# Kernel tuning notes

Hardware: AMD Instinct MI355X
Metric: run time of the kernel (lower is better)

## Reference

```python
import jax, jax.numpy as jnp
import numpy as np

B, K = 16384, 32      # batch nodes, sampled neighbors per node
N, F, E = 1000000, 128, 128  # table size, feature_dim, embed_dim


def setup_inputs() -> dict:
    key = jax.random.key(0)
    k1, k2, k3 = jax.random.split(key, 3)
    id2feat = jax.random.normal(k1, (N, F), dtype=jnp.float32)
    # xavier_uniform for weight
    limit = float(np.sqrt(6.0 / (F + E)))
    weight = jax.random.uniform(k2, (F, E), dtype=jnp.float32, minval=-limit, maxval=limit)
    bias = jnp.zeros((E,), dtype=jnp.float32)
    neigh_idx = jax.random.randint(k3, (B, K), 0, N, dtype=jnp.int64)
    return {"id2feat": id2feat, "weight": weight, "bias": bias, "neigh_idx": neigh_idx}


def reference(id2feat, weight, bias, neigh_idx):
    # gather neighbor features: [B, K, F]
    feats = id2feat[neigh_idx]
    # linear transform then mean over neighbors (== mask.mm(embed_matrix))
    emb = jnp.einsum('bkf,fe->bke', feats, weight) + bias  # [B, K, E]
    return emb.mean(axis=1)  # [B, E]
```

## Files before the change

### kernel.cpp

```cpp
#include <hip/hip_runtime.h>


#define BATCH 16384
#define KNB   32
#define FDIM  128
#define EDIM  128
#define ROWS_PER_BLOCK 16
#define IDX_PITCH 33
#define A_PITCH  132

__global__ __launch_bounds__(256, 2)
void spa_agg_kernel(const float* __restrict__ id2feat,
                    const float* __restrict__ weight,
                    const float* __restrict__ bias,
                    const int* __restrict__ neigh_idx,
                    float* __restrict__ out) {
    __shared__ float sW[FDIM * EDIM];
    __shared__ float sA[ROWS_PER_BLOCK * A_PITCH];
    __shared__ int   sIdx[ROWS_PER_BLOCK * IDX_PITCH];

    const int tid = threadIdx.x;
    const int lb  = tid >> 4;
    const int fg  = tid & 15;
    const int b0  = blockIdx.x * ROWS_PER_BLOCK;

    {
        const int base = b0 * KNB;
        for (int i = tid; i < ROWS_PER_BLOCK * KNB; i += 256) {
            int r = i >> 5, c = i & 31;
            sIdx[r * IDX_PITCH + c] = neigh_idx[base + i];
        }
    }
    {
        for (int i = tid; i < (FDIM * EDIM) / 4; i += 256) {
            int f = i >> 5, e4 = i & 31;
            const float4 w = *(const float4*)(weight + (size_t)f * EDIM + e4 * 4);
            *(float4*)&sW[f * 128 + (e4 & 1) * 64 + (e4 >> 1) * 4] = w;
        }
    }
    __syncthreads();

    {
        float acc[8];
        #pragma unroll
        for (int j = 0; j < 8; ++j) acc[j] = 0.f;
        const int* ip = &sIdx[lb * IDX_PITCH];
        #pragma unroll 8
        for (int k = 0; k < KNB; ++k) {
            const int row = ip[k];
            const float4* rp = (const float4*)(id2feat + (size_t)row * FDIM + fg * 8);
            const float4 r0 = rp[0];
            const float4 r1 = rp[1];
            acc[0] += r0.x; acc[1] += r0.y; acc[2] += r0.z; acc[3] += r0.w;
            acc[4] += r1.x; acc[5] += r1.y; acc[6] += r1.z; acc[7] += r1.w;
        }
        float* ap = &sA[lb * A_PITCH + fg * 8];
        #pragma unroll
        for (int j = 0; j < 8; ++j) ap[j] = acc[j] * (1.f / 32.f);
    }
    __syncthreads();

    {
        const int e0 = fg * 8;
        float acc[8];
        #pragma unroll
        for (int j = 0; j < 8; ++j) acc[j] = bias[e0 + j];
        const float* arow = &sA[lb * A_PITCH];
        #pragma unroll 4
        for (int f = 0; f < FDIM; ++f) {
            const float a   = arow[f];
            const float4 w0 = *(const float4*)&sW[f * 128 + fg * 4];
            const float4 w1 = *(const float4*)&sW[f * 128 + 64 + fg * 4];
            acc[0] += a * w0.x; acc[1] += a * w0.y;
            acc[2] += a * w0.z; acc[3] += a * w0.w;
            acc[4] += a * w1.x; acc[5] += a * w1.y;
            acc[6] += a * w1.z; acc[7] += a * w1.w;
        }
        float* op = out + (size_t)(b0 + lb) * EDIM + e0;
        *(float4*)op       = make_float4(acc[0], acc[1], acc[2], acc[3]);
        *(float4*)(op + 4) = make_float4(acc[4], acc[5], acc[6], acc[7]);
    }
}

extern "C" void kernel_launch(void* const* d_in, const int* in_sizes, int n_in,
                              void* d_out, int out_size, void* d_ws, size_t ws_size,
                              hipStream_t stream) {
    const float* id2feat = (const float*)d_in[0];
    const float* weight  = (const float*)d_in[1];
    const float* bias    = (const float*)d_in[2];
    const int*   neigh   = (const int*)d_in[3];
    float*       outp    = (float*)d_out;

    dim3 grid(BATCH / ROWS_PER_BLOCK);
    dim3 block(256);
    spa_agg_kernel<<<grid, block, 0, stream>>>(id2feat, weight, bias, neigh, outp);
}
```

Measured before the change: 607.5 us.

## Drop shared weight staging and halve rows per block for higher occupancy

The 64 KB shared-memory copy of the weight matrix is removed, and the GEMV stage now reads weight rows straight from global memory through the cache. Rows per block drop to 8, and each warp of 32 threads handles one batch row with a float4 per lane. With shared memory nearly empty, the launch bounds now allow 6 blocks per CU, giving more loads in flight for the random gather. The cost is that every block reads the full weight from L2/L1 instead of LDS, and twice as many blocks are launched.

Result: no change. 614.1 us (+1.1%).

```diff
diff --git a/kernel.cpp b/kernel.cpp
--- a/kernel.cpp
+++ b/kernel.cpp
@@ -5,80 +5,59 @@
 #define KNB   32
 #define FDIM  128
 #define EDIM  128
-#define ROWS_PER_BLOCK 16
+#define ROWS_PER_BLOCK 8
 #define IDX_PITCH 33
 #define A_PITCH  132
 
-__global__ __launch_bounds__(256, 2)
+__global__ __launch_bounds__(256, 6)
 void spa_agg_kernel(const float* __restrict__ id2feat,
                     const float* __restrict__ weight,
                     const float* __restrict__ bias,
                     const int* __restrict__ neigh_idx,
                     float* __restrict__ out) {
-    __shared__ float sW[FDIM * EDIM];
     __shared__ float sA[ROWS_PER_BLOCK * A_PITCH];
     __shared__ int   sIdx[ROWS_PER_BLOCK * IDX_PITCH];
 
     const int tid = threadIdx.x;
-    const int lb  = tid >> 4;
-    const int fg  = tid & 15;
+    const int lr  = tid >> 5;
+    const int c   = tid & 31;
     const int b0  = blockIdx.x * ROWS_PER_BLOCK;
 
     {
-        const int base = b0 * KNB;
-        for (int i = tid; i < ROWS_PER_BLOCK * KNB; i += 256) {
-            int r = i >> 5, c = i & 31;
-            sIdx[r * IDX_PITCH + c] = neigh_idx[base + i];
-        }
-    }
-    {
-        for (int i = tid; i < (FDIM * EDIM) / 4; i += 256) {
-            int f = i >> 5, e4 = i & 31;
-            const float4 w = *(const float4*)(weight + (size_t)f * EDIM + e4 * 4);
-            *(float4*)&sW[f * 128 + (e4 & 1) * 64 + (e4 >> 1) * 4] = w;
-        }
+        const int i = tid;
+        sIdx[(i >> 5) * IDX_PITCH + (i & 31)] = neigh_idx[b0 * KNB + i];
     }
     __syncthreads();
 
     {
-        float acc[8];
-        #pragma unroll
-        for (int j = 0; j < 8; ++j) acc[j] = 0.f;
-        const int* ip = &sIdx[lb * IDX_PITCH];
+        float4 acc = make_float4(0.f, 0.f, 0.f, 0.f);
+        const int* ip = &sIdx[lr * IDX_PITCH];
         #pragma unroll 8
         for (int k = 0; k < KNB; ++k) {
             const int row = ip[k];
-            const float4* rp = (const float4*)(id2feat + (size_t)row * FDIM + fg * 8);
-            const float4 r0 = rp[0];
-            const float4 r1 = rp[1];
-            acc[0] += r0.x; acc[1] += r0.y; acc[2] += r0.z; acc[3] += r0.w;
-            acc[4] += r1.x; acc[5] += r1.y; acc[6] += r1.z; acc[7] += r1.w;
+            const float4 r = *(const float4*)(id2feat + (size_t)row * FDIM + c * 4);
+            acc.x += r.x; acc.y += r.y; acc.z += r.z; acc.w += r.w;
         }
-        float* ap = &sA[lb * A_PITCH + fg * 8];
-        #pragma unroll
-        for (int j = 0; j < 8; ++j) ap[j] = acc[j] * (1.f / 32.f);
+        float* ap = &sA[lr * A_PITCH + c * 4];
+        ap[0] = acc.x * (1.f / 32.f);
+        ap[1] = acc.y * (1.f / 32.f);
+        ap[2] = acc.z * (1.f / 32.f);
+        ap[3] = acc.w * (1.f / 32.f);
     }
     __syncthreads();
 
     {
-        const int e0 = fg * 8;
-        float acc[8];
-        #pragma unroll
-        for (int j = 0; j < 8; ++j) acc[j] = bias[e0 + j];
-        const float* arow = &sA[lb * A_PITCH];
+        const int e0 = c * 4;
+        float4 acc = *(const float4*)(bias + e0);
+        const float* arow = &sA[lr * A_PITCH];
         #pragma unroll 4
         for (int f = 0; f < FDIM; ++f) {
-            const float a   = arow[f];
-            const float4 w0 = *(const float4*)&sW[f * 128 + fg * 4];
-            const float4 w1 = *(const float4*)&sW[f * 128 + 64 + fg * 4];
-            acc[0] += a * w0.x; acc[1] += a * w0.y;
-            acc[2] += a * w0.z; acc[3] += a * w0.w;
-            acc[4] += a * w1.x; acc[5] += a * w1.y;
-            acc[6] += a * w1.z; acc[7] += a * w1.w;
+            const float  a = arow[f];
+            const float4 w = *(const float4*)(weight + (size_t)f * EDIM + e0);
+            acc.x += a * w.x; acc.y += a * w.y;
+            acc.z += a * w.z; acc.w += a * w.w;
         }
-        float* op = out + (size_t)(b0 + lb) * EDIM + e0;
-        *(float4*)op       = make_float4(acc[0], acc[1], acc[2], acc[3]);
-        *(float4*)(op + 4) = make_float4(acc[4], acc[5], acc[6], acc[7]);
+        *(float4*)(out + (size_t)(b0 + lr) * EDIM + e0) = acc;
     }
 }
 
```
